# Kernel tuning notes

Measured on AMD Instinct MI355X. Metric: run time of the kernel, lower is better.

The kernel has to match this reference:

```python
import jax, jax.numpy as jnp
import numpy as np

N_NODES = 100000
N_EDGES = 3200000
N_GRAPHS = 1024
D_IN, D_HID, N_CLASSES = 128, 64, 10


def setup_inputs() -> dict:
    key = jax.random.key(0)
    ks = jax.random.split(key, 12)
    x = jax.random.normal(ks[0], (N_NODES, D_IN), dtype=jnp.float32)
    edge_index = jax.random.randint(ks[1], (2, N_EDGES), 0, N_NODES, dtype=jnp.int64)
    batch = jnp.sort(jax.random.randint(ks[2], (N_NODES,), 0, N_GRAPHS, dtype=jnp.int64))
    def w(k, shape, fan_in):
        return (jax.random.normal(k, shape, dtype=jnp.float32) / np.sqrt(fan_in)).astype(jnp.float32)
    return {
        "x": x,
        "edge_index": edge_index,
        "batch": batch,
        "W1": w(ks[3], (D_IN, D_HID), D_IN),  "b1": jnp.zeros((D_HID,), jnp.float32),
        "W2": w(ks[4], (D_HID, D_HID), D_HID), "b2": jnp.zeros((D_HID,), jnp.float32),
        "W3": w(ks[5], (D_HID, D_HID), D_HID), "b3": jnp.zeros((D_HID,), jnp.float32),
        "Wl": w(ks[6], (D_HID, N_CLASSES), D_HID), "bl": jnp.zeros((N_CLASSES,), jnp.float32),
    }


def _gcn_conv(x, W, b, src, dst, n_nodes):
    # GCNConv: out = D^{-1/2} (A + I) D^{-1/2} X W + b  (symmetric norm, self-loops)
    h = x @ W  # [N, D_out] - transform first (PyG order)
    loop = jnp.arange(n_nodes, dtype=src.dtype)
    s = jnp.concatenate([src, loop])  # [E+N]
    d = jnp.concatenate([dst, loop])
    deg = jax.ops.segment_sum(jnp.ones_like(d, dtype=h.dtype), d, num_segments=n_nodes)
    dinv = jnp.where(deg > 0, jax.lax.rsqrt(deg), 0.0)
    norm = dinv[s] * dinv[d]  # [E+N]
    out = jax.ops.segment_sum(h[s] * norm[:, None], d, num_segments=n_nodes)
    return out + b


def reference(x, edge_index, batch, W1, b1, W2, b2, W3, b3, Wl, bl):
    src, dst = edge_index[0], edge_index[1]
    n = x.shape[0]
    h = jax.nn.relu(_gcn_conv(x, W1, b1, src, dst, n))
    h = jax.nn.relu(_gcn_conv(h, W2, b2, src, dst, n))
    h = _gcn_conv(h, W3, b3, src, dst, n)
    # global mean pool over graphs
    sums = jax.ops.segment_sum(h, batch, num_segments=N_GRAPHS)
    cnts = jax.ops.segment_sum(jnp.ones((n,), h.dtype), batch, num_segments=N_GRAPHS)
    g = sums / jnp.maximum(cnts, 1.0)[:, None]
    # dropout is identity in eval mode
    return g @ Wl + bl  # [N_GRAPHS, N_CLASSES]
```

## Files before the change

kernel.cpp:

```cpp
#include <hip/hip_runtime.h>
#include <hip/hip_fp16.h>

#define D_IN 128
#define D_HID 64
#define N_GRAPHS 1024
#define N_CLASSES 10

#define NPB 256
#define MAXNB 1024
#define CHUNK 16384

typedef __attribute__((ext_vector_type(8))) short bf16x8;
typedef __attribute__((ext_vector_type(4))) float f32x4;

__device__ __forceinline__ unsigned bf16_rne(float f) {
    unsigned u = __float_as_uint(f);
    return (u + 0x7FFF + ((u >> 16) & 1)) >> 16;
}

__global__ __launch_bounds__(256) void hist_buckets(const int* __restrict__ dst, int nE, int NB,
                                                    int* __restrict__ bcnt) {
    __shared__ int h[MAXNB];
    for (int i = threadIdx.x; i < NB; i += 256) h[i] = 0;
    __syncthreads();
    int stride = gridDim.x * 256;
    for (int i = blockIdx.x * 256 + threadIdx.x; i < nE; i += stride)
        atomicAdd(&h[dst[i] >> 8], 1);
    __syncthreads();
    for (int i = threadIdx.x; i < NB; i += 256) {
        int c = h[i];
        if (c) atomicAdd(&bcnt[i], c);
    }
}

template <int K>
__device__ void pack_dev(const float* __restrict__ W, short* __restrict__ hi, short* __restrict__ lo) {
    constexpr int SLOTS = (K / 32) * 4 * 64;
    for (int s = threadIdx.x; s < SLOTS; s += 1024) {
        int lane = s & 63, nf = (s >> 6) & 3, ks = s >> 8;
        int fq = lane >> 4, fr = lane & 15;
#pragma unroll
        for (int j = 0; j < 8; ++j) {
            int k = ks * 32 + fq * 8 + j;
            int c = nf * 16 + fr;
            float v = W[k * 64 + c];
            unsigned hb = bf16_rne(v);
            float hf = __uint_as_float(hb << 16);
            float l = v - hf;
            hi[s * 8 + j] = (short)hb;
            lo[s * 8 + j] = (short)bf16_rne(l);
        }
    }
}

__global__ __launch_bounds__(1024) void fused_prep(
    const int* __restrict__ bcnt, int NB, int nE,
    int* __restrict__ boff, int* __restrict__ gcur,
    const float* __restrict__ W1, short* __restrict__ w1hi, short* __restrict__ w1lo,
    const float* __restrict__ W2, short* __restrict__ w2hi, short* __restrict__ w2lo,
    const float* __restrict__ W3, short* __restrict__ w3hi, short* __restrict__ w3lo,
    float* __restrict__ sums, float* __restrict__ gcnt) {
    __shared__ int t[1024];
    int b = blockIdx.x, tid = threadIdx.x;
    if (b == 0) {
        int v = (tid < NB) ? bcnt[tid] : 0;
        t[tid] = v;
        __syncthreads();
        for (int off = 1; off < 1024; off <<= 1) {
            int u = (tid >= off) ? t[tid - off] : 0;
            __syncthreads();
            t[tid] += u;
            __syncthreads();
        }
        int excl = t[tid] - v;
        if (tid < NB) { boff[tid] = excl; gcur[tid] = excl; }
        if (tid == 0) boff[NB] = nE;
    } else if (b == 1) {
        pack_dev<D_IN>(W1, w1hi, w1lo);
    } else if (b == 2) {
        pack_dev<D_HID>(W2, w2hi, w2lo);
    } else if (b == 3) {
        pack_dev<D_HID>(W3, w3hi, w3lo);
    } else {
        const int total = N_GRAPHS * 64;
        for (int i = (b - 4) * 1024 + tid; i < total; i += 8 * 1024) sums[i] = 0.0f;
        for (int i = (b - 4) * 1024 + tid; i < N_GRAPHS; i += 8 * 1024) gcnt[i] = 0.0f;
    }
}

__global__ __launch_bounds__(1024) void bin_edges(const int* __restrict__ src, const int* __restrict__ dst,
                                                  int nE, int NB, int* __restrict__ gcur,
                                                  int* __restrict__ binned) {
    __shared__ int h[MAXNB];
    __shared__ int base[MAXNB];
    int c0 = blockIdx.x * CHUNK;
    int c1 = min(nE, c0 + CHUNK);
    for (int i = threadIdx.x; i < NB; i += 1024) h[i] = 0;
    __syncthreads();
    for (int i = c0 + threadIdx.x; i < c1; i += 1024) atomicAdd(&h[dst[i] >> 8], 1);
    __syncthreads();
    for (int b = threadIdx.x; b < NB; b += 1024) {
        int c = h[b];
        base[b] = c ? atomicAdd(&gcur[b], c) : 0;
        h[b] = 0;
    }
    __syncthreads();
    for (int i = c0 + threadIdx.x; i < c1; i += 1024) {
        int d = dst[i];
        int b = d >> 8;
        int r = atomicAdd(&h[b], 1);
        binned[base[b] + r] = src[i] | ((d & 255) << 17);
    }
}

__global__ __launch_bounds__(256) void build_csr(const int* __restrict__ boff,
                                                 const int* __restrict__ binned,
                                                 int n, int nE,
                                                 int* __restrict__ rowptr, float* __restrict__ dinv,
                                                 int* __restrict__ csr_src) {
    __shared__ int cnt[NPB];
    __shared__ int soff[NPB];
    __shared__ int cur[NPB];
    int b = blockIdx.x, tid = threadIdx.x;
    int nbase = b << 8;
    int e0 = boff[b], e1 = boff[b + 1];
    cnt[tid] = 0;
    __syncthreads();
    for (int i = e0 + tid; i < e1; i += 256) atomicAdd(&cnt[binned[i] >> 17], 1);
    __syncthreads();
    int v = cnt[tid];
    soff[tid] = v;
    __syncthreads();
    for (int off = 1; off < 256; off <<= 1) {
        int u = (tid >= off) ? soff[tid - off] : 0;
        __syncthreads();
        soff[tid] += u;
        __syncthreads();
    }
    int excl = soff[tid] - v;
    __syncthreads();
    soff[tid] = excl;
    cur[tid] = 0;
    int node = nbase + tid;
    if (node < n) {
        rowptr[node] = e0 + excl;
        dinv[node] = 1.0f / sqrtf((float)(cnt[tid] + 1));
    }
    if (b == 0 && tid == 0) rowptr[n] = nE;
    __syncthreads();
    for (int i = e0 + tid; i < e1; i += 256) {
        int e = binned[i];
        int ld = e >> 17;
        int r = atomicAdd(&cur[ld], 1);
        csr_src[e0 + soff[ld] + r] = e & 0x1FFFF;
    }
}

template <int K>
__global__ __launch_bounds__(256) void gemm_mfma(
    const float* __restrict__ X, const short* __restrict__ whi, const short* __restrict__ wlo,
    const float* __restrict__ bias, int relu, __half* __restrict__ H, int n) {
    constexpr int KS = K / 32;
    int wave = threadIdx.x >> 6, lane = threadIdx.x & 63;
    int fr = lane & 15, fq = lane >> 4;
    int rowbase = blockIdx.x * 64 + wave * 16;
    int rclamp = min(rowbase + fr, n - 1);
    f32x4 acc[4] = {{0,0,0,0},{0,0,0,0},{0,0,0,0},{0,0,0,0}};
#pragma unroll
    for (int ks = 0; ks < KS; ++ks) {
        const float* xp = X + (size_t)rclamp * K + ks * 32 + fq * 8;
        float xv[8];
        *(f32x4*)&xv[0] = *(const f32x4*)xp;
        *(f32x4*)&xv[4] = *(const f32x4*)(xp + 4);
        if (bias != nullptr) {
            const float* bp = bias + ks * 32 + fq * 8;
#pragma unroll
            for (int j = 0; j < 8; ++j) {
                float v = xv[j] + bp[j];
                if (relu) v = fmaxf(v, 0.0f);
                xv[j] = v;
            }
        }
        bf16x8 ahi, alo;
#pragma unroll
        for (int j = 0; j < 8; ++j) {
            unsigned hb = bf16_rne(xv[j]);
            float hf = __uint_as_float(hb << 16);
            ahi[j] = (short)hb;
            alo[j] = (short)bf16_rne(xv[j] - hf);
        }
        const short* whp = whi + (size_t)(ks * 4) * 64 * 8 + lane * 8;
        const short* wlp = wlo + (size_t)(ks * 4) * 64 * 8 + lane * 8;
#pragma unroll
        for (int nf = 0; nf < 4; ++nf) {
            bf16x8 bhi = *(const bf16x8*)(whp + nf * 512);
            bf16x8 blo = *(const bf16x8*)(wlp + nf * 512);
            acc[nf] = __builtin_amdgcn_mfma_f32_16x16x32_bf16(ahi, bhi, acc[nf], 0, 0, 0);
            acc[nf] = __builtin_amdgcn_mfma_f32_16x16x32_bf16(alo, bhi, acc[nf], 0, 0, 0);
            acc[nf] = __builtin_amdgcn_mfma_f32_16x16x32_bf16(ahi, blo, acc[nf], 0, 0, 0);
        }
    }
#pragma unroll
    for (int nf = 0; nf < 4; ++nf) {
#pragma unroll
        for (int reg = 0; reg < 4; ++reg) {
            int r = rowbase + fq * 4 + reg;
            if (r < n) H[((size_t)r << 6) + nf * 16 + fr] = __float2half(acc[nf][reg]);
        }
    }
}

__global__ __launch_bounds__(256) void gather_agg(
    const int* __restrict__ rowptr, const int* __restrict__ csr_src,
    const float* __restrict__ dinv, const __half* __restrict__ A,
    float* __restrict__ B, int n) {
    int gtid = blockIdx.x * 256 + threadIdx.x;
    int wid = gtid >> 6, lane = gtid & 63;
    int nw = (gridDim.x * 256) >> 6;
    int slot = lane >> 3, fl = lane & 7;
    for (int d = wid; d < n; d += nw) {
        float dd = dinv[d];
        int e0 = rowptr[d], e1 = rowptr[d + 1];
        float acc[8];
#pragma unroll
        for (int j = 0; j < 8; ++j) acc[j] = 0.0f;
        if (slot == 0) {
            uint4 q = *(const uint4*)(A + ((size_t)d << 6) + (fl << 3));
            const __half2* hp = (const __half2*)&q;
            float w = dd * dd;
#pragma unroll
            for (int j = 0; j < 4; ++j) {
                float2 f = __half22float2(hp[j]);
                acc[2 * j] = w * f.x;
                acc[2 * j + 1] = w * f.y;
            }
        }
        int e = e0 + slot;
        for (; e + 8 < e1; e += 16) {
            int s0 = csr_src[e], s1 = csr_src[e + 8];
            float w0 = dd * dinv[s0], w1 = dd * dinv[s1];
            uint4 q0 = *(const uint4*)(A + ((size_t)s0 << 6) + (fl << 3));
            uint4 q1 = *(const uint4*)(A + ((size_t)s1 << 6) + (fl << 3));
            const __half2* h0 = (const __half2*)&q0;
            const __half2* h1 = (const __half2*)&q1;
#pragma unroll
            for (int j = 0; j < 4; ++j) {
                float2 f0 = __half22float2(h0[j]);
                float2 f1 = __half22float2(h1[j]);
                acc[2 * j]     = fmaf(w0, f0.x, acc[2 * j]);
                acc[2 * j + 1] = fmaf(w0, f0.y, acc[2 * j + 1]);
                acc[2 * j]     = fmaf(w1, f1.x, acc[2 * j]);
                acc[2 * j + 1] = fmaf(w1, f1.y, acc[2 * j + 1]);
            }
        }
        if (e < e1) {
            int s = csr_src[e];
            float w = dd * dinv[s];
            uint4 q = *(const uint4*)(A + ((size_t)s << 6) + (fl << 3));
            const __half2* hp = (const __half2*)&q;
#pragma unroll
            for (int j = 0; j < 4; ++j) {
                float2 f = __half22float2(hp[j]);
                acc[2 * j]     = fmaf(w, f.x, acc[2 * j]);
                acc[2 * j + 1] = fmaf(w, f.y, acc[2 * j + 1]);
            }
        }
#pragma unroll
        for (int m = 8; m <= 32; m <<= 1)
#pragma unroll
            for (int j = 0; j < 8; ++j) acc[j] += __shfl_xor(acc[j], m);
        if (slot == 0) {
            float* bp = B + ((size_t)d << 6) + (fl << 3);
            *(f32x4*)bp = *(f32x4*)&acc[0];
            *(f32x4*)(bp + 4) = *(f32x4*)&acc[4];
        }
    }
}

__global__ __launch_bounds__(256) void pool_nodes(
    const float* __restrict__ B, const float* __restrict__ b3,
    const int* __restrict__ batch, float* __restrict__ sums,
    float* __restrict__ gcnt, int n, int chunk) {
    int gtid = blockIdx.x * blockDim.x + threadIdx.x;
    int wid = gtid >> 6, lane = gtid & 63;
    int start = wid * chunk;
    if (start >= n) return;
    int end = min(n, start + chunk);
    float bl3 = b3[lane];
    int curg = batch[start];
    float acc = 0.0f;
    int cl = 0;
    for (int node = start; node < end; ++node) {
        int g = batch[node];
        if (g != curg) {
            atomicAdd(&sums[((size_t)curg << 6) + lane], acc);
            if (lane == 0) atomicAdd(&gcnt[curg], (float)cl);
            acc = 0.0f; cl = 0; curg = g;
        }
        acc += B[((size_t)node << 6) + lane] + bl3;
        ++cl;
    }
    atomicAdd(&sums[((size_t)curg << 6) + lane], acc);
    if (lane == 0) atomicAdd(&gcnt[curg], (float)cl);
}

__global__ void final_linear(const float* __restrict__ sums, const float* __restrict__ gcnt,
                             const float* __restrict__ Wl, const float* __restrict__ bl,
                             float* __restrict__ out) {
    int idx = blockIdx.x * blockDim.x + threadIdx.x;
    if (idx >= N_GRAPHS * N_CLASSES) return;
    int g = idx / N_CLASSES, c = idx - g * N_CLASSES;
    float inv = 1.0f / fmaxf(gcnt[g], 1.0f);
    float acc = bl[c];
#pragma unroll
    for (int d = 0; d < D_HID; ++d)
        acc = fmaf(sums[(g << 6) + d] * inv, Wl[d * N_CLASSES + c], acc);
    out[idx] = acc;
}

extern "C" void kernel_launch(void* const* d_in, const int* in_sizes, int n_in,
                              void* d_out, int out_size, void* d_ws, size_t ws_size,
                              hipStream_t stream) {
    const float* x     = (const float*)d_in[0];
    const int*   ei    = (const int*)d_in[1];
    const int*   batch = (const int*)d_in[2];
    const float* W1 = (const float*)d_in[3];
    const float* b1 = (const float*)d_in[4];
    const float* W2 = (const float*)d_in[5];
    const float* b2 = (const float*)d_in[6];
    const float* W3 = (const float*)d_in[7];
    const float* b3 = (const float*)d_in[8];
    const float* Wl = (const float*)d_in[9];
    const float* bl = (const float*)d_in[10];

    int n = in_sizes[0] / D_IN;
    int E = in_sizes[1] / 2;
    const int* src = ei;
    const int* dst = ei + E;
    int NB = (n + NPB - 1) / NPB;

    size_t off = 0;
    auto alloc = [&](size_t bytes) {
        void* p = (char*)d_ws + off;
        off += ((bytes + 255) & ~(size_t)255);
        return p;
    };
    int*    rowptr  = (int*)alloc(((size_t)n + 1) * 4);
    int*    bcnt    = (int*)alloc(MAXNB * 4);
    int*    boff    = (int*)alloc((MAXNB + 1) * 4);
    int*    gcur    = (int*)alloc(MAXNB * 4);
    int*    binned  = (int*)alloc((size_t)E * 4);
    int*    csr_src = (int*)alloc((size_t)E * 4);
    float*  dinv    = (float*)alloc((size_t)n * 4);
    float*  B       = (float*)alloc((size_t)n * 64 * 4);
    float*  sums    = (float*)alloc(N_GRAPHS * 64 * 4);
    float*  gcnt    = (float*)alloc(N_GRAPHS * 4);
    short*  w1hi    = (short*)alloc(4 * 4 * 64 * 8 * 2);
    short*  w1lo    = (short*)alloc(4 * 4 * 64 * 8 * 2);
    short*  w2hi    = (short*)alloc(2 * 4 * 64 * 8 * 2);
    short*  w2lo    = (short*)alloc(2 * 4 * 64 * 8 * 2);
    short*  w3hi    = (short*)alloc(2 * 4 * 64 * 8 * 2);
    short*  w3lo    = (short*)alloc(2 * 4 * 64 * 8 * 2);
    __half* A       = (__half*)binned;

    int blk = 256;
    int gBin  = (E + CHUNK - 1) / CHUNK;
    int gGemm = (n + 63) / 64;

    hipMemsetAsync(bcnt, 0, MAXNB * sizeof(int), stream);
    hist_buckets<<<1024, blk, 0, stream>>>(dst, E, NB, bcnt);
    fused_prep<<<12, 1024, 0, stream>>>(bcnt, NB, E, boff, gcur,
                                        W1, w1hi, w1lo, W2, w2hi, w2lo, W3, w3hi, w3lo,
                                        sums, gcnt);
    bin_edges<<<gBin, 1024, 0, stream>>>(src, dst, E, NB, gcur, binned);
    build_csr<<<NB, blk, 0, stream>>>(boff, binned, n, E, rowptr, dinv, csr_src);

    gemm_mfma<D_IN><<<gGemm, blk, 0, stream>>>(x, w1hi, w1lo, nullptr, 0, A, n);
    gather_agg<<<2048, blk, 0, stream>>>(rowptr, csr_src, dinv, A, B, n);

    gemm_mfma<D_HID><<<gGemm, blk, 0, stream>>>(B, w2hi, w2lo, b1, 1, A, n);
    gather_agg<<<2048, blk, 0, stream>>>(rowptr, csr_src, dinv, A, B, n);

    gemm_mfma<D_HID><<<gGemm, blk, 0, stream>>>(B, w3hi, w3lo, b2, 1, A, n);
    gather_agg<<<2048, blk, 0, stream>>>(rowptr, csr_src, dinv, A, B, n);

    {
        int waves = 256 * 256 / 64;
        int chunk = (n + waves - 1) / waves;
        pool_nodes<<<256, blk, 0, stream>>>(B, b3, batch, sums, gcnt, n, chunk);
    }
    final_linear<<<(N_GRAPHS * N_CLASSES + blk - 1) / blk, blk, 0, stream>>>(
        sums, gcnt, Wl, bl, (float*)d_out);
}
```

Measured before the change: 349.7 us.

## Fuse aggregation with next-layer GEMM and fuse final aggregation into pooling

```diff
diff --git a/kernel.cpp b/kernel.cpp
--- a/kernel.cpp
+++ b/kernel.cpp
@@ -9,6 +9,7 @@
 #define NPB 256
 #define MAXNB 1024
 #define CHUNK 16384
+#define XS_STRIDE 68
 
 typedef __attribute__((ext_vector_type(8))) short bf16x8;
 typedef __attribute__((ext_vector_type(4))) float f32x4;
@@ -159,7 +160,7 @@
 template <int K>
 __global__ __launch_bounds__(256) void gemm_mfma(
     const float* __restrict__ X, const short* __restrict__ whi, const short* __restrict__ wlo,
-    const float* __restrict__ bias, int relu, __half* __restrict__ H, int n) {
+    __half* __restrict__ H, int n) {
     constexpr int KS = K / 32;
     int wave = threadIdx.x >> 6, lane = threadIdx.x & 63;
     int fr = lane & 15, fq = lane >> 4;
@@ -172,15 +173,6 @@
         float xv[8];
         *(f32x4*)&xv[0] = *(const f32x4*)xp;
         *(f32x4*)&xv[4] = *(const f32x4*)(xp + 4);
-        if (bias != nullptr) {
-            const float* bp = bias + ks * 32 + fq * 8;
-#pragma unroll
-            for (int j = 0; j < 8; ++j) {
-                float v = xv[j] + bp[j];
-                if (relu) v = fmaxf(v, 0.0f);
-                xv[j] = v;
-            }
-        }
         bf16x8 ahi, alo;
 #pragma unroll
         for (int j = 0; j < 8; ++j) {
@@ -210,10 +202,124 @@
     }
 }
 
-__global__ __launch_bounds__(256) void gather_agg(
+__global__ __launch_bounds__(256) void gather_gemm(
     const int* __restrict__ rowptr, const int* __restrict__ csr_src,
     const float* __restrict__ dinv, const __half* __restrict__ A,
-    float* __restrict__ B, int n) {
+    const short* __restrict__ whi, const short* __restrict__ wlo,
+    const float* __restrict__ bias, __half* __restrict__ Hout, int n) {
+    __shared__ float xs[64 * XS_STRIDE];
+    int tid = threadIdx.x;
+    int wave = tid >> 6, lane = tid & 63;
+    int slot = lane >> 3, fl = lane & 7;
+    int rowbase = blockIdx.x * 64;
+    for (int i = 0; i < 16; ++i) {
+        int lr = (wave << 4) + i;
+        int d = rowbase + lr;
+        float acc[8];
+#pragma unroll
+        for (int j = 0; j < 8; ++j) acc[j] = 0.0f;
+        if (d < n) {
+            float dd = dinv[d];
+            int e0 = rowptr[d], e1 = rowptr[d + 1];
+            if (slot == 0) {
+                uint4 q = *(const uint4*)(A + ((size_t)d << 6) + (fl << 3));
+                const __half2* hp = (const __half2*)&q;
+                float w = dd * dd;
+#pragma unroll
+                for (int j = 0; j < 4; ++j) {
+                    float2 f = __half22float2(hp[j]);
+                    acc[2 * j] = w * f.x;
+                    acc[2 * j + 1] = w * f.y;
+                }
+            }
+            int e = e0 + slot;
+            for (; e + 8 < e1; e += 16) {
+                int s0 = csr_src[e], s1 = csr_src[e + 8];
+                float w0 = dd * dinv[s0], w1 = dd * dinv[s1];
+                uint4 q0 = *(const uint4*)(A + ((size_t)s0 << 6) + (fl << 3));
+                uint4 q1 = *(const uint4*)(A + ((size_t)s1 << 6) + (fl << 3));
+                const __half2* h0 = (const __half2*)&q0;
+                const __half2* h1 = (const __half2*)&q1;
+#pragma unroll
+                for (int j = 0; j < 4; ++j) {
+                    float2 f0 = __half22float2(h0[j]);
+                    float2 f1 = __half22float2(h1[j]);
+                    acc[2 * j]     = fmaf(w0, f0.x, acc[2 * j]);
+                    acc[2 * j + 1] = fmaf(w0, f0.y, acc[2 * j + 1]);
+                    acc[2 * j]     = fmaf(w1, f1.x, acc[2 * j]);
+                    acc[2 * j + 1] = fmaf(w1, f1.y, acc[2 * j + 1]);
+                }
+            }
+            if (e < e1) {
+                int s = csr_src[e];
+                float w = dd * dinv[s];
+                uint4 q = *(const uint4*)(A + ((size_t)s << 6) + (fl << 3));
+                const __half2* hp = (const __half2*)&q;
+#pragma unroll
+                for (int j = 0; j < 4; ++j) {
+                    float2 f = __half22float2(hp[j]);
+                    acc[2 * j]     = fmaf(w, f.x, acc[2 * j]);
+                    acc[2 * j + 1] = fmaf(w, f.y, acc[2 * j + 1]);
+                }
+            }
+#pragma unroll
+            for (int m = 8; m <= 32; m <<= 1)
+#pragma unroll
+                for (int j = 0; j < 8; ++j) acc[j] += __shfl_xor(acc[j], m);
+        }
+        if (slot == 0) {
+            float* xp = &xs[lr * XS_STRIDE + (fl << 3)];
+            *(f32x4*)xp = *(f32x4*)&acc[0];
+            *(f32x4*)(xp + 4) = *(f32x4*)&acc[4];
+        }
+    }
+    __syncthreads();
+    int fr = lane & 15, fq = lane >> 4;
+    f32x4 acc4[4] = {{0,0,0,0},{0,0,0,0},{0,0,0,0},{0,0,0,0}};
+#pragma unroll
+    for (int ks = 0; ks < 2; ++ks) {
+        int kbase = ks * 32 + fq * 8;
+        const float* xp = &xs[((wave << 4) + fr) * XS_STRIDE + kbase];
+        float xv[8];
+        *(f32x4*)&xv[0] = *(const f32x4*)xp;
+        *(f32x4*)&xv[4] = *(const f32x4*)(xp + 4);
+        const float* bp = bias + kbase;
+#pragma unroll
+        for (int j = 0; j < 8; ++j) xv[j] = fmaxf(xv[j] + bp[j], 0.0f);
+        bf16x8 ahi, alo;
+#pragma unroll
+        for (int j = 0; j < 8; ++j) {
+            unsigned hb = bf16_rne(xv[j]);
+            float hf = __uint_as_float(hb << 16);
+            ahi[j] = (short)hb;
+            alo[j] = (short)bf16_rne(xv[j] - hf);
+        }
+        const short* whp = whi + (size_t)(ks * 4) * 64 * 8 + lane * 8;
+        const short* wlp = wlo + (size_t)(ks * 4) * 64 * 8 + lane * 8;
+#pragma unroll
+        for (int nf = 0; nf < 4; ++nf) {
+            bf16x8 bhi = *(const bf16x8*)(whp + nf * 512);
+            bf16x8 blo = *(const bf16x8*)(wlp + nf * 512);
+            acc4[nf] = __builtin_amdgcn_mfma_f32_16x16x32_bf16(ahi, bhi, acc4[nf], 0, 0, 0);
+            acc4[nf] = __builtin_amdgcn_mfma_f32_16x16x32_bf16(alo, bhi, acc4[nf], 0, 0, 0);
+            acc4[nf] = __builtin_amdgcn_mfma_f32_16x16x32_bf16(ahi, blo, acc4[nf], 0, 0, 0);
+        }
+    }
+#pragma unroll
+    for (int nf = 0; nf < 4; ++nf) {
+#pragma unroll
+        for (int reg = 0; reg < 4; ++reg) {
+            int r = rowbase + (wave << 4) + fq * 4 + reg;
+            if (r < n) Hout[((size_t)r << 6) + nf * 16 + fr] = __float2half(acc4[nf][reg]);
+        }
+    }
+}
+
+__global__ __launch_bounds__(256) void gather_pool(
+    const int* __restrict__ rowptr, const int* __restrict__ csr_src,
+    const float* __restrict__ dinv, const __half* __restrict__ A,
+    const int* __restrict__ batch, float* __restrict__ sums,
+    float* __restrict__ gcnt, int n) {
     int gtid = blockIdx.x * 256 + threadIdx.x;
     int wid = gtid >> 6, lane = gtid & 63;
     int nw = (gridDim.x * 256) >> 6;
@@ -270,41 +376,17 @@
 #pragma unroll
             for (int j = 0; j < 8; ++j) acc[j] += __shfl_xor(acc[j], m);
         if (slot == 0) {
-            float* bp = B + ((size_t)d << 6) + (fl << 3);
-            *(f32x4*)bp = *(f32x4*)&acc[0];
-            *(f32x4*)(bp + 4) = *(f32x4*)&acc[4];
-        }
-    }
-}
-
-__global__ __launch_bounds__(256) void pool_nodes(
-    const float* __restrict__ B, const float* __restrict__ b3,
-    const int* __restrict__ batch, float* __restrict__ sums,
-    float* __restrict__ gcnt, int n, int chunk) {
-    int gtid = blockIdx.x * blockDim.x + threadIdx.x;
-    int wid = gtid >> 6, lane = gtid & 63;
-    int start = wid * chunk;
-    if (start >= n) return;
-    int end = min(n, start + chunk);
-    float bl3 = b3[lane];
-    int curg = batch[start];
-    float acc = 0.0f;
-    int cl = 0;
-    for (int node = start; node < end; ++node) {
-        int g = batch[node];
-        if (g != curg) {
-            atomicAdd(&sums[((size_t)curg << 6) + lane], acc);
-            if (lane == 0) atomicAdd(&gcnt[curg], (float)cl);
-            acc = 0.0f; cl = 0; curg = g;
-        }
-        acc += B[((size_t)node << 6) + lane] + bl3;
-        ++cl;
-    }
-    atomicAdd(&sums[((size_t)curg << 6) + lane], acc);
-    if (lane == 0) atomicAdd(&gcnt[curg], (float)cl);
+            int g = batch[d];
+            float* sp = &sums[((size_t)g << 6) + (fl << 3)];
+#pragma unroll
+            for (int j = 0; j < 8; ++j) atomicAdd(sp + j, acc[j]);
+            if (fl == 0) atomicAdd(&gcnt[g], 1.0f);
+        }
+    }
 }
 
 __global__ void final_linear(const float* __restrict__ sums, const float* __restrict__ gcnt,
+                             const float* __restrict__ b3,
                              const float* __restrict__ Wl, const float* __restrict__ bl,
                              float* __restrict__ out) {
     int idx = blockIdx.x * blockDim.x + threadIdx.x;
@@ -314,7 +396,7 @@
     float acc = bl[c];
 #pragma unroll
     for (int d = 0; d < D_HID; ++d)
-        acc = fmaf(sums[(g << 6) + d] * inv, Wl[d * N_CLASSES + c], acc);
+        acc = fmaf(sums[(g << 6) + d] * inv + b3[d], Wl[d * N_CLASSES + c], acc);
     out[idx] = acc;
 }
 
@@ -352,7 +434,7 @@
     int*    binned  = (int*)alloc((size_t)E * 4);
     int*    csr_src = (int*)alloc((size_t)E * 4);
     float*  dinv    = (float*)alloc((size_t)n * 4);
-    float*  B       = (float*)alloc((size_t)n * 64 * 4);
+    __half* C       = (__half*)alloc((size_t)n * 64 * 2);
     float*  sums    = (float*)alloc(N_GRAPHS * 64 * 4);
     float*  gcnt    = (float*)alloc(N_GRAPHS * 4);
     short*  w1hi    = (short*)alloc(4 * 4 * 64 * 8 * 2);
@@ -375,20 +457,14 @@
     bin_edges<<<gBin, 1024, 0, stream>>>(src, dst, E, NB, gcur, binned);
     build_csr<<<NB, blk, 0, stream>>>(boff, binned, n, E, rowptr, dinv, csr_src);
 
-    gemm_mfma<D_IN><<<gGemm, blk, 0, stream>>>(x, w1hi, w1lo, nullptr, 0, A, n);
-    gather_agg<<<2048, blk, 0, stream>>>(rowptr, csr_src, dinv, A, B, n);
-
-    gemm_mfma<D_HID><<<gGemm, blk, 0, stream>>>(B, w2hi, w2lo, b1, 1, A, n);
-    gather_agg<<<2048, blk, 0, stream>>>(rowptr, csr_src, dinv, A, B, n);
-
-    gemm_mfma<D_HID><<<gGemm, blk, 0, stream>>>(B, w3hi, w3lo, b2, 1, A, n);
-    gather_agg<<<2048, blk, 0, stream>>>(rowptr, csr_src, dinv, A, B, n);
-
-    {
-        int waves = 256 * 256 / 64;
-        int chunk = (n + waves - 1) / waves;
-        pool_nodes<<<256, blk, 0, stream>>>(B, b3, batch, sums, gcnt, n, chunk);
-    }
+    gemm_mfma<D_IN><<<gGemm, blk, 0, stream>>>(x, w1hi, w1lo, A, n);
+
+    gather_gemm<<<gGemm, blk, 0, stream>>>(rowptr, csr_src, dinv, A, w2hi, w2lo, b1, C, n);
+
+    gather_gemm<<<gGemm, blk, 0, stream>>>(rowptr, csr_src, dinv, C, w3hi, w3lo, b2, A, n);
+
+    gather_pool<<<2048, blk, 0, stream>>>(rowptr, csr_src, dinv, A, batch, sums, gcnt, n);
+
     final_linear<<<(N_GRAPHS * N_CLASSES + blk - 1) / blk, blk, 0, stream>>>(
-        sums, gcnt, Wl, bl, (float*)d_out);
-}
+        sums, gcnt, b3, Wl, bl, (float*)d_out);
+}
```

New measurement: 621.3 us. +77.7%, slower.
